# Performance work log

Hardware: AMD Instinct MI355X
Metric: run time of the kernel (lower is better)

Reference implementation:

```python
import jax, jax.numpy as jnp
import numpy as np

C = 256          # conv_channels
C1 = C // 2      # 128
C2 = C // 4      # 64
G = 1            # relation_glimpse


def setup_inputs() -> dict:
    key = jax.random.key(0)
    ks = jax.random.split(key, 20)
    bs, Nr, in_dim, q_dim = 4, 256, 2052, 1024
    d_in = in_dim + 4  # pos (first 4 coords) re-appended
    s = 0.02
    inp = {
        "Q": jax.random.normal(ks[0], (bs, q_dim), jnp.float32),
        "X": jax.random.normal(ks[1], (bs, Nr, in_dim), jnp.float32),
        "Wv": jax.random.normal(ks[2], (d_in, C), jnp.float32) * s,
        "bv": jnp.zeros((C,), jnp.float32),
        "Wq": jax.random.normal(ks[3], (q_dim, C), jnp.float32) * s,
        "bq": jnp.zeros((C,), jnp.float32),
        # branch 0 (r_conv01/02/03): 1x1 convs == per-position dense
        "W01": jax.random.normal(ks[4], (C, C1), jnp.float32) * s,
        "b01": jnp.zeros((C1,), jnp.float32),
        "W02": jax.random.normal(ks[5], (C1, C2), jnp.float32) * s,
        "b02": jnp.zeros((C2,), jnp.float32),
        "W03": jax.random.normal(ks[6], (C2, G), jnp.float32) * s,
        "b03": jnp.zeros((G,), jnp.float32),
        # branch 1 (r_conv1/2/3): dilation on 1x1 kernels is a no-op
        "W1": jax.random.normal(ks[7], (C, C1), jnp.float32) * s,
        "b1": jnp.zeros((C1,), jnp.float32),
        "W2": jax.random.normal(ks[8], (C1, C2), jnp.float32) * s,
        "b2": jnp.zeros((C2,), jnp.float32),
        "W3": jax.random.normal(ks[9], (C2, G), jnp.float32) * s,
        "b3": jnp.zeros((G,), jnp.float32),
    }
    return inp


def _mlp3(P, Wa, ba, Wb, bb, Wc, bc):
    # P: [bs, Nr, Nr, C]; three 1x1-conv layers, ReLU after each (incl. last).
    h = jax.nn.relu(jnp.einsum("bijc,ck->bijk", P, Wa) + ba)
    h = jax.nn.relu(jnp.einsum("bijc,ck->bijk", h, Wb) + bb)
    h = jax.nn.relu(jnp.einsum("bijc,ck->bijk", h, Wc) + bc)
    return h[..., 0]  # [bs, Nr, Nr] (relation_glimpse == 1)


def _attn_map(h):
    # symmetrize, then softmax over all Nr*Nr positions
    s = h + jnp.swapaxes(h, 1, 2)
    bs, Nr, _ = s.shape
    return jax.nn.softmax(s.reshape(bs, Nr * Nr), axis=-1).reshape(bs, Nr, Nr)


def reference(Q, X, Wv, bv, Wq, bq, W01, b01, W02, b02, W03, b03,
              W1, b1, W2, b2, W3, b3):
    X_ = X
    # append pos (first 4 coords) -> [bs, Nr, in_dim+4]
    Xcat = jnp.concatenate([X, X[:, :, :4]], axis=2)
    Xp = jnp.einsum("bnd,dc->bnc", Xcat, Wv) + bv
    Qp = Q @ Wq + bq
    Xp = Xp + Qp[:, None, :]                       # [bs, Nr, C]
    P = Xp[:, None, :, :] * Xp[:, :, None, :]      # [bs, Nr, Nr, C] pairwise product
    m0 = _attn_map(_mlp3(P, W01, b01, W02, b02, W03, b03))
    m1 = _attn_map(_mlp3(P, W1, b1, W2, b2, W3, b3))
    # weighted aggregation with original features; /(2*glimpse), then sum over Nr
    rel = jnp.einsum("bij,bjd->bid", m0 + m1, X_) / (2.0 * G)
    return rel.sum(axis=1)  # [bs, in_dim]
```

## Files before the change

kernel.cpp:

```cpp
#include <hip/hip_runtime.h>
#include <hip/hip_bf16.h>

typedef __attribute__((ext_vector_type(8)))  short short8;
typedef __attribute__((ext_vector_type(4)))  float f32x4;
typedef __attribute__((ext_vector_type(16))) float f32x16;

#define NR 256
#define CC 256

__device__ __forceinline__ unsigned short f2bf(float x) {
    union { float f; unsigned int u; } v; v.f = x;
    unsigned int r = v.u + 0x7FFFu + ((v.u >> 16) & 1u);
    return (unsigned short)(r >> 16);
}

__device__ __forceinline__ unsigned int pk2bf(float a, float b) {
    __hip_bfloat162 h = __float22bfloat162_rn(make_float2(a, b));
    union { __hip_bfloat162 h; unsigned int u; } cv; cv.h = h;
    return cv.u;
}

__global__ __launch_bounds__(256) void setup_kernel(
    const float* __restrict__ Q, const float* __restrict__ Wq, float* __restrict__ Qpp,
    const float* __restrict__ Wv, unsigned short* __restrict__ wvp,
    const float* __restrict__ W01, const float* __restrict__ W1,
    const float* __restrict__ W02, const float* __restrict__ W2,
    unsigned short* __restrict__ wpa, unsigned short* __restrict__ wpb)
{
    __shared__ float tile[32][260];
    __shared__ float qs[256];
    const int bx = blockIdx.x;
    const int tid = threadIdx.x;

    if (bx < 16) {
        int ksl = bx & 3, b = bx >> 2;
        qs[tid] = Q[b * 1024 + ksl * 256 + tid];
        __syncthreads();
        float acc = 0.f;
        #pragma unroll 4
        for (int d = 0; d < 256; ++d) acc += qs[d] * Wq[(size_t)(ksl * 256 + d) * 256 + tid];
        Qpp[(ksl * 4 + b) * 256 + tid] = acc;
    } else if (bx < 81) {
        int ks = bx - 16;
        for (int idx = tid; idx < 32 * 256; idx += 256) {
            int cr = idx >> 8, n = idx & 255;
            int c = ks * 32 + cr;
            tile[cr][n] = (c < 2056) ? Wv[(size_t)c * 256 + n] : 0.f;
        }
        __syncthreads();
        #pragma unroll
        for (int q = 0; q < 4; ++q) {
            int t2 = tid * 4 + q;
            int nt = t2 >> 6, l = t2 & 63;
            int gg = l >> 4, jj = l & 15;
            short8 s;
            #pragma unroll
            for (int e = 0; e < 8; ++e)
                s[e] = (short)f2bf(tile[gg * 8 + e][nt * 16 + jj]);
            *(short8*)&wvp[((size_t)(ks * 16 + nt) * 64 + l) * 8] = s;
        }
    } else {
        int t = (bx - 81) * 256 + tid;
        if (t < 65536) {
            int e = t & 7, l = (t >> 3) & 63, ks = (t >> 9) & 15, nt = (t >> 13) & 3, br = (t >> 15) & 1;
            int cc = ks * 16 + (l >> 5) * 8 + e;
            int n = nt * 32 + (l & 31);
            const float* W = br ? W1 : W01;
            wpa[t] = f2bf(W[cc * 128 + n]);
        } else {
            int t2 = t - 65536;
            int e = t2 & 7, l = (t2 >> 3) & 63, ks = (t2 >> 9) & 7, nt = (t2 >> 12) & 1, br = (t2 >> 13) & 1;
            int cc = ks * 16 + (l >> 5) * 8 + e;
            int n = nt * 32 + (l & 31);
            const float* W = br ? W2 : W02;
            wpb[t2] = f2bf(W[cc * 64 + n]);
        }
    }
}

__global__ __launch_bounds__(512) void xp_kernel(
    const float* __restrict__ X, const unsigned short* __restrict__ wvp,
    const float* __restrict__ bv, const float* __restrict__ bq,
    const float* __restrict__ Qpp, float* __restrict__ Xp)
{
    __shared__ f32x4 red[8][2][65];
    const int tid = threadIdx.x;
    const int w = tid >> 6;
    const int lane = tid & 63;
    const int g = lane >> 4, j16 = lane & 15;
    const int mt = blockIdx.x;
    const int bn = blockIdx.y;
    const int b  = blockIdx.z;

    const int i0 = mt * 16;
    const int n0 = bn * 32;
    const float* xrow = X + ((size_t)(b * NR) + (i0 + j16)) * 2052;

    f32x4 acc[2] = {};

    for (int ks = w; ks < 64; ks += 8) {
        const int c0 = ks * 32 + g * 8;
        float4 xa = *(const float4*)(xrow + c0);
        float4 xb = *(const float4*)(xrow + c0 + 4);
        union { short8 s; unsigned int u[4]; } af;
        af.u[0] = pk2bf(xa.x, xa.y);
        af.u[1] = pk2bf(xa.z, xa.w);
        af.u[2] = pk2bf(xb.x, xb.y);
        af.u[3] = pk2bf(xb.z, xb.w);
        #pragma unroll
        for (int nt = 0; nt < 2; ++nt) {
            short8 bf = ((const short8*)wvp)[(size_t)(ks * 16 + bn * 2 + nt) * 64 + lane];
            acc[nt] = __builtin_amdgcn_mfma_f32_16x16x32_bf16(af.s, bf, acc[nt], 0, 0, 0);
        }
    }
    if (w == 0) {
        float xv[8];
        #pragma unroll
        for (int e = 0; e < 8; ++e) {
            int q = g * 8 + e;
            int csrc = (q < 4) ? (2048 + q) : (q - 4);
            xv[e] = xrow[csrc];
        }
        union { short8 s; unsigned int u[4]; } af;
        af.u[0] = pk2bf(xv[0], xv[1]);
        af.u[1] = pk2bf(xv[2], xv[3]);
        af.u[2] = pk2bf(xv[4], xv[5]);
        af.u[3] = pk2bf(xv[6], xv[7]);
        #pragma unroll
        for (int nt = 0; nt < 2; ++nt) {
            short8 bf = ((const short8*)wvp)[(size_t)(64 * 16 + bn * 2 + nt) * 64 + lane];
            acc[nt] = __builtin_amdgcn_mfma_f32_16x16x32_bf16(af.s, bf, acc[nt], 0, 0, 0);
        }
    }
    #pragma unroll
    for (int nt = 0; nt < 2; ++nt) red[w][nt][lane] = acc[nt];
    __syncthreads();

    {
        int nt  = tid >> 8;
        int rem = tid & 255;
        int l   = rem & 63;
        int reg = (rem >> 6) & 3;
        float r = 0.f;
        #pragma unroll
        for (int ww = 0; ww < 8; ++ww) r += red[ww][nt][l][reg];
        int gg = l >> 4, jj = l & 15;
        int n = n0 + nt * 16 + jj;
        float base = bv[n] + bq[n] + Qpp[b * 256 + n] + Qpp[(4 + b) * 256 + n]
                   + Qpp[(8 + b) * 256 + n] + Qpp[(12 + b) * 256 + n];
        int row = i0 + gg * 4 + reg;
        Xp[((b * NR) + row) * CC + n] = r + base;
    }
}

__global__ __launch_bounds__(512, 2) void pairs_kernel(
    const float* __restrict__ Xp,
    const unsigned short* __restrict__ wpa,
    const unsigned short* __restrict__ wpb,
    const float* __restrict__ b01, const float* __restrict__ b02,
    const float* __restrict__ b03,
    const float* __restrict__ b1,  const float* __restrict__ b2,
    const float* __restrict__ b3,
    const float* __restrict__ W03, const float* __restrict__ W3,
    float* __restrict__ colpart, float* __restrict__ rowpart)
{
    __shared__ __align__(16) unsigned short lds_wa[32768];
    __shared__ __align__(16) float lds_si[2048];
    __shared__ __align__(16) float lds_bias1[128];
    __shared__ __align__(16) float lds_bias2[64];
    __shared__ __align__(16) float lds_w3[64];
    __shared__ float lds_c[8][33];

    const int tid = threadIdx.x;
    const int wave = tid >> 6;
    const int lane = tid & 63;
    const int hi = lane >> 5;
    const int j32 = lane & 31;

    int bx = blockIdx.x;
    int b = bx / 288;
    int r = bx - b * 288;
    int br = r / 144;
    int u = r - br * 144;
    int k = 0, off = 0;
    while (k < 7) {
        int cnt = 4 * (8 - k);
        if (u < off + cnt) break;
        off += cnt; ++k;
    }
    int rel = u - off;
    int it8 = 4 * k + rel / (8 - k);
    int jt  = k + rel % (8 - k);

    const int i = it8 * 8 + wave;
    const int blk = br * 4 + b;
    const int j0 = jt * 32;
    const int j = j0 + j32;

    *(float4*)&lds_si[wave * 256 + lane * 4] =
        *(const float4*)&Xp[((b * NR) + i) * CC + lane * 4];

    {
        const uint4* g1 = (const uint4*)(wpa + (size_t)br * 32768);
        uint4* s1 = (uint4*)lds_wa;
        #pragma unroll
        for (int kk = 0; kk < 8; ++kk) s1[kk * 512 + tid] = g1[kk * 512 + tid];
        if (tid < 128) lds_bias1[tid] = br ? b1[tid] : b01[tid];
        else if (tid < 192) lds_bias2[tid - 128] = br ? b2[tid - 128] : b02[tid - 128];
        else if (tid < 256) lds_w3[tid - 192] = br ? W3[tid - 192] : W03[tid - 192];
    }
    __syncthreads();
    const float b3v = br ? b3[0] : b03[0];
    const float* si = lds_si + wave * 256;

    const float* xr = Xp + ((size_t)(b * NR) + j) * CC;
    short8 bfr[16];
    #pragma unroll
    for (int ks = 0; ks < 16; ++ks) {
        const int c0 = ks * 16 + hi * 8;
        float4 xa = *(const float4*)(xr + c0);
        float4 xb = *(const float4*)(xr + c0 + 4);
        float4 sa = *(const float4*)(si + c0);
        float4 sb = *(const float4*)(si + c0 + 4);
        union { short8 s; unsigned int uu[4]; } f;
        f.uu[0] = pk2bf(xa.x * sa.x, xa.y * sa.y);
        f.uu[1] = pk2bf(xa.z * sa.z, xa.w * sa.w);
        f.uu[2] = pk2bf(xb.x * sb.x, xb.y * sb.y);
        f.uu[3] = pk2bf(xb.z * sb.z, xb.w * sb.w);
        bfr[ks] = f.s;
    }

    f32x16 acc1[4];
    #pragma unroll
    for (int t = 0; t < 4; ++t) {
        #pragma unroll
        for (int q = 0; q < 4; ++q) {
            const float* bb = &lds_bias1[t * 32 + q * 8 + hi * 4];
            acc1[t][q * 4 + 0] = bb[0];
            acc1[t][q * 4 + 1] = bb[1];
            acc1[t][q * 4 + 2] = bb[2];
            acc1[t][q * 4 + 3] = bb[3];
        }
    }
    #pragma unroll
    for (int ks = 0; ks < 16; ++ks) {
        const short8 bb = bfr[ks];
        #pragma unroll
        for (int t = 0; t < 4; ++t) {
            short8 wf = ((const short8*)lds_wa)[(t * 16 + ks) * 64 + lane];
            acc1[t] = __builtin_amdgcn_mfma_f32_32x32x16_bf16(wf, bb, acc1[t], 0, 0, 0);
        }
    }

    short8 w2r[16];
    {
        const short8* wb = (const short8*)wpb + (size_t)br * 1024;
        #pragma unroll
        for (int q = 0; q < 16; ++q) w2r[q] = wb[q * 64 + lane];
    }

    f32x16 acc2[2];
    #pragma unroll
    for (int nt = 0; nt < 2; ++nt) {
        #pragma unroll
        for (int q = 0; q < 4; ++q) {
            const float* bb = &lds_bias2[nt * 32 + q * 8 + hi * 4];
            acc2[nt][q * 4 + 0] = bb[0];
            acc2[nt][q * 4 + 1] = bb[1];
            acc2[nt][q * 4 + 2] = bb[2];
            acc2[nt][q * 4 + 3] = bb[3];
        }
    }
    #pragma unroll
    for (int t = 0; t < 4; ++t) {
        #pragma unroll
        for (int s = 0; s < 2; ++s) {
            const int bse = s * 8;
            float rA0 = fmaxf(acc1[t][bse + 0], 0.f), rA1 = fmaxf(acc1[t][bse + 1], 0.f);
            float rA2 = fmaxf(acc1[t][bse + 2], 0.f), rA3 = fmaxf(acc1[t][bse + 3], 0.f);
            float rB0 = fmaxf(acc1[t][bse + 4], 0.f), rB1 = fmaxf(acc1[t][bse + 5], 0.f);
            float rB2 = fmaxf(acc1[t][bse + 6], 0.f), rB3 = fmaxf(acc1[t][bse + 7], 0.f);
            unsigned int uA0 = pk2bf(rA0, rA1), uA1 = pk2bf(rA2, rA3);
            unsigned int uB0 = pk2bf(rB0, rB1), uB1 = pk2bf(rB2, rB3);
            unsigned int pA0 = __shfl_xor(uA0, 32, 64), pA1 = __shfl_xor(uA1, 32, 64);
            unsigned int pB0 = __shfl_xor(uB0, 32, 64), pB1 = __shfl_xor(uB1, 32, 64);
            union { short8 s8; unsigned int uu[4]; } B2;
            B2.uu[0] = hi ? pB0 : uA0;
            B2.uu[1] = hi ? pB1 : uA1;
            B2.uu[2] = hi ? uB0 : pA0;
            B2.uu[3] = hi ? uB1 : pA1;
            const int ks2 = 2 * t + s;
            acc2[0] = __builtin_amdgcn_mfma_f32_32x32x16_bf16(w2r[ks2], B2.s8, acc2[0], 0, 0, 0);
            acc2[1] = __builtin_amdgcn_mfma_f32_32x32x16_bf16(w2r[8 + ks2], B2.s8, acc2[1], 0, 0, 0);
        }
    }

    float part = 0.f;
    #pragma unroll
    for (int nt = 0; nt < 2; ++nt) {
        #pragma unroll
        for (int q = 0; q < 4; ++q) {
            const float* wv = &lds_w3[nt * 32 + q * 8 + hi * 4];
            part += fmaxf(acc2[nt][q * 4 + 0], 0.f) * wv[0];
            part += fmaxf(acc2[nt][q * 4 + 1], 0.f) * wv[1];
            part += fmaxf(acc2[nt][q * 4 + 2], 0.f) * wv[2];
            part += fmaxf(acc2[nt][q * 4 + 3], 0.f) * wv[3];
        }
    }
    part += __shfl_xor(part, 32, 64);
    const float h3 = fmaxf(part + b3v, 0.f);
    const float E = __expf(2.f * h3);
    const float Ec = (j >= i) ? E : 0.f;
    float Er = (j >  i) ? E : 0.f;

    Er += __shfl_xor(Er, 1, 64);
    Er += __shfl_xor(Er, 2, 64);
    Er += __shfl_xor(Er, 4, 64);
    Er += __shfl_xor(Er, 8, 64);
    Er += __shfl_xor(Er, 16, 64);
    Er += __shfl_xor(Er, 32, 64);
    if (lane == 0)
        rowpart[((size_t)blk * NR + i) * 8 + jt] = 0.5f * Er;

    if (!hi) lds_c[wave][j32] = Ec;
    __syncthreads();
    if (tid < 32) {
        float c = 0.f;
        #pragma unroll
        for (int w2 = 0; w2 < 8; ++w2) c += lds_c[w2][tid];
        colpart[(size_t)blk * 4608 + 64 * jt * (jt + 1) + tid * (4 * jt + 4) + it8] = c;
    }
}

__global__ __launch_bounds__(256) void colsoft_final_kernel(
    const float* __restrict__ colpart, const float* __restrict__ rowpart,
    float* __restrict__ wn)
{
    const int blk = blockIdx.x;
    const int j = threadIdx.x;
    const int jt = j >> 5, j32l = j & 31;
    const int cnt = 4 * jt + 4;
    float cs = 0.f;
    const float* cp = colpart + (size_t)blk * 4608 + 64 * jt * (jt + 1) + j32l * cnt;
    for (int it2 = 0; it2 < cnt; ++it2) cs += cp[it2];
    const float* rp = rowpart + ((size_t)blk * NR + j) * 8;
    for (int q = jt; q < 8; ++q) cs += rp[q];

    __shared__ float red[256];
    red[j] = cs; __syncthreads();
    for (int s = 128; s > 0; s >>= 1) {
        if (j < s) red[j] += red[j + s];
        __syncthreads();
    }
    wn[blk * 256 + j] = cs / red[0];
}

__global__ __launch_bounds__(256) void agg_part_kernel(
    const float* __restrict__ X, const float* __restrict__ wn,
    float* __restrict__ apart)
{
    const int dc = blockIdx.x, b = blockIdx.y, jc = blockIdx.z;
    const int d = dc * 256 + threadIdx.x;
    __shared__ float wc[32];
    if (threadIdx.x < 32) {
        int j = jc * 32 + threadIdx.x;
        wc[threadIdx.x] = 0.5f * (wn[b * 256 + j] + wn[(4 + b) * 256 + j]);
    }
    __syncthreads();
    if (d < 2052) {
        const float* xp = X + (size_t)b * NR * 2052 + (size_t)jc * 32 * 2052 + d;
        float a0 = 0.f, a1 = 0.f, a2 = 0.f, a3 = 0.f;
        for (int rr = 0; rr < 32; rr += 4) {
            a0 += wc[rr + 0] * xp[(size_t)(rr + 0) * 2052];
            a1 += wc[rr + 1] * xp[(size_t)(rr + 1) * 2052];
            a2 += wc[rr + 2] * xp[(size_t)(rr + 2) * 2052];
            a3 += wc[rr + 3] * xp[(size_t)(rr + 3) * 2052];
        }
        apart[(size_t)(jc * 4 + b) * 2304 + d] = (a0 + a1) + (a2 + a3);
    }
}

__global__ __launch_bounds__(256) void agg_final_kernel(
    const float* __restrict__ apart, float* __restrict__ out)
{
    const int dc = blockIdx.x, b = blockIdx.y;
    const int d = dc * 256 + threadIdx.x;
    if (d < 2052) {
        float s = 0.f;
        #pragma unroll
        for (int jc = 0; jc < 8; ++jc) s += apart[(size_t)(jc * 4 + b) * 2304 + d];
        out[b * 2052 + d] = s;
    }
}

extern "C" void kernel_launch(void* const* d_in, const int* in_sizes, int n_in,
                              void* d_out, int out_size, void* d_ws, size_t ws_size,
                              hipStream_t stream) {
    const float* Q   = (const float*)d_in[0];
    const float* X   = (const float*)d_in[1];
    const float* Wv  = (const float*)d_in[2];
    const float* bv  = (const float*)d_in[3];
    const float* Wq  = (const float*)d_in[4];
    const float* bq  = (const float*)d_in[5];
    const float* W01 = (const float*)d_in[6];
    const float* b01 = (const float*)d_in[7];
    const float* W02 = (const float*)d_in[8];
    const float* b02 = (const float*)d_in[9];
    const float* W03 = (const float*)d_in[10];
    const float* b03 = (const float*)d_in[11];
    const float* W1  = (const float*)d_in[12];
    const float* b1  = (const float*)d_in[13];
    const float* W2  = (const float*)d_in[14];
    const float* b2  = (const float*)d_in[15];
    const float* W3  = (const float*)d_in[16];
    const float* b3  = (const float*)d_in[17];

    char* ws = (char*)d_ws;
    float* Xp   = (float*)(ws + 0);
    float* Qpp  = (float*)(ws + 1048576);
    float* wn   = (float*)(ws + 1064960);
    unsigned short* wpa = (unsigned short*)(ws + 1073152);
    unsigned short* wpb = (unsigned short*)(ws + 1204224);
    float* colpart = (float*)(ws + 1236992);
    float* rowpart = (float*)(ws + 1384448);
    unsigned short* wvp = (unsigned short*)(ws + 1236992);
    float* apart = (float*)(ws + 0);
    float* out = (float*)d_out;

    setup_kernel<<<401, 256, 0, stream>>>(Q, Wq, Qpp, Wv, wvp,
                                          W01, W1, W02, W2, wpa, wpb);
    xp_kernel<<<dim3(16, 8, 4), 512, 0, stream>>>(X, wvp, bv, bq, Qpp, Xp);
    pairs_kernel<<<1152, 512, 0, stream>>>(Xp, wpa, wpb, b01, b02, b03,
                                           b1, b2, b3, W03, W3, colpart, rowpart);
    colsoft_final_kernel<<<8, 256, 0, stream>>>(colpart, rowpart, wn);
    agg_part_kernel<<<dim3(9, 4, 8), 256, 0, stream>>>(X, wn, apart);
    agg_final_kernel<<<dim3(9, 4), 256, 0, stream>>>(apart, out);
}
```

Measured before the change: 91.93 us.

## Switch pairs MLP to 16x16 MFMA tiles, merge softmax normalization into aggregation

The pairs kernel now uses 16x16x32 MFMA with 16-column j tiles instead of 32x32x16. It streams the first-layer weights into LDS in two halves and keeps the second-layer weights in LDS rather than registers, which shrinks LDS and register footprint and doubles the block count. The xp kernel computes 128 output columns per block (fewer blocks, more reuse of X loads). The separate column-softmax kernel is removed and its normalization is recomputed redundantly inside each aggregation block, saving one launch at the cost of duplicated reductions.

```diff
diff --git a/kernel.cpp b/kernel.cpp
--- a/kernel.cpp
+++ b/kernel.cpp
@@ -3,7 +3,6 @@
 
 typedef __attribute__((ext_vector_type(8)))  short short8;
 typedef __attribute__((ext_vector_type(4)))  float f32x4;
-typedef __attribute__((ext_vector_type(16))) float f32x16;
 
 #define NR 256
 #define CC 256
@@ -62,16 +61,16 @@
     } else {
         int t = (bx - 81) * 256 + tid;
         if (t < 65536) {
-            int e = t & 7, l = (t >> 3) & 63, ks = (t >> 9) & 15, nt = (t >> 13) & 3, br = (t >> 15) & 1;
-            int cc = ks * 16 + (l >> 5) * 8 + e;
-            int n = nt * 32 + (l & 31);
+            int e = t & 7, l = (t >> 3) & 63, ks = (t >> 9) & 7, nt = (t >> 12) & 7, br = (t >> 15) & 1;
+            int cc = ks * 32 + (l >> 4) * 8 + e;
+            int n = nt * 16 + (l & 15);
             const float* W = br ? W1 : W01;
             wpa[t] = f2bf(W[cc * 128 + n]);
         } else {
             int t2 = t - 65536;
-            int e = t2 & 7, l = (t2 >> 3) & 63, ks = (t2 >> 9) & 7, nt = (t2 >> 12) & 1, br = (t2 >> 13) & 1;
-            int cc = ks * 16 + (l >> 5) * 8 + e;
-            int n = nt * 32 + (l & 31);
+            int e = t2 & 7, l = (t2 >> 3) & 63, ks = (t2 >> 9) & 3, nt = (t2 >> 11) & 3, br = (t2 >> 13) & 1;
+            int cc = ks * 32 + (l >> 4) * 8 + e;
+            int n = nt * 16 + (l & 15);
             const float* W = br ? W2 : W02;
             wpb[t2] = f2bf(W[cc * 64 + n]);
         }
@@ -83,20 +82,19 @@
     const float* __restrict__ bv, const float* __restrict__ bq,
     const float* __restrict__ Qpp, float* __restrict__ Xp)
 {
-    __shared__ f32x4 red[8][2][65];
+    __shared__ f32x4 red[8][8][65];
     const int tid = threadIdx.x;
     const int w = tid >> 6;
     const int lane = tid & 63;
-    const int g = lane >> 4, j16 = lane & 15;
+    const int g = lane >> 4, j16v = lane & 15;
     const int mt = blockIdx.x;
-    const int bn = blockIdx.y;
+    const int bn2 = blockIdx.y;
     const int b  = blockIdx.z;
 
     const int i0 = mt * 16;
-    const int n0 = bn * 32;
-    const float* xrow = X + ((size_t)(b * NR) + (i0 + j16)) * 2052;
-
-    f32x4 acc[2] = {};
+    const float* xrow = X + ((size_t)(b * NR) + (i0 + j16v)) * 2052;
+
+    f32x4 acc[8] = {};
 
     for (int ks = w; ks < 64; ks += 8) {
         const int c0 = ks * 32 + g * 8;
@@ -108,8 +106,8 @@
         af.u[2] = pk2bf(xb.x, xb.y);
         af.u[3] = pk2bf(xb.z, xb.w);
         #pragma unroll
-        for (int nt = 0; nt < 2; ++nt) {
-            short8 bf = ((const short8*)wvp)[(size_t)(ks * 16 + bn * 2 + nt) * 64 + lane];
+        for (int nt = 0; nt < 8; ++nt) {
+            short8 bf = ((const short8*)wvp)[(size_t)(ks * 16 + bn2 * 8 + nt) * 64 + lane];
             acc[nt] = __builtin_amdgcn_mfma_f32_16x16x32_bf16(af.s, bf, acc[nt], 0, 0, 0);
         }
     }
@@ -127,29 +125,27 @@
         af.u[2] = pk2bf(xv[4], xv[5]);
         af.u[3] = pk2bf(xv[6], xv[7]);
         #pragma unroll
-        for (int nt = 0; nt < 2; ++nt) {
-            short8 bf = ((const short8*)wvp)[(size_t)(64 * 16 + bn * 2 + nt) * 64 + lane];
+        for (int nt = 0; nt < 8; ++nt) {
+            short8 bf = ((const short8*)wvp)[(size_t)(64 * 16 + bn2 * 8 + nt) * 64 + lane];
             acc[nt] = __builtin_amdgcn_mfma_f32_16x16x32_bf16(af.s, bf, acc[nt], 0, 0, 0);
         }
     }
     #pragma unroll
-    for (int nt = 0; nt < 2; ++nt) red[w][nt][lane] = acc[nt];
-    __syncthreads();
-
-    {
-        int nt  = tid >> 8;
-        int rem = tid & 255;
-        int l   = rem & 63;
-        int reg = (rem >> 6) & 3;
-        float r = 0.f;
-        #pragma unroll
-        for (int ww = 0; ww < 8; ++ww) r += red[ww][nt][l][reg];
+    for (int nt = 0; nt < 8; ++nt) red[w][nt][lane] = acc[nt];
+    __syncthreads();
+
+    for (int idx = tid; idx < 2048; idx += 512) {
+        int nt = idx >> 8, rem = idx & 255;
+        int l = rem & 63, reg = rem >> 6;
+        float rsum = 0.f;
+        #pragma unroll
+        for (int ww = 0; ww < 8; ++ww) rsum += red[ww][nt][l][reg];
         int gg = l >> 4, jj = l & 15;
-        int n = n0 + nt * 16 + jj;
+        int n = bn2 * 128 + nt * 16 + jj;
         float base = bv[n] + bq[n] + Qpp[b * 256 + n] + Qpp[(4 + b) * 256 + n]
                    + Qpp[(8 + b) * 256 + n] + Qpp[(12 + b) * 256 + n];
         int row = i0 + gg * 4 + reg;
-        Xp[((b * NR) + row) * CC + n] = r + base;
+        Xp[((b * NR) + row) * CC + n] = rsum + base;
     }
 }
 
@@ -164,60 +160,68 @@
     const float* __restrict__ W03, const float* __restrict__ W3,
     float* __restrict__ colpart, float* __restrict__ rowpart)
 {
-    __shared__ __align__(16) unsigned short lds_wa[32768];
+    __shared__ __align__(16) unsigned short lds_wa[16384];
+    __shared__ __align__(16) unsigned short lds_wb[8192];
     __shared__ __align__(16) float lds_si[2048];
     __shared__ __align__(16) float lds_bias1[128];
     __shared__ __align__(16) float lds_bias2[64];
     __shared__ __align__(16) float lds_w3[64];
-    __shared__ float lds_c[8][33];
+    __shared__ float lds_c[8][17];
 
     const int tid = threadIdx.x;
     const int wave = tid >> 6;
     const int lane = tid & 63;
-    const int hi = lane >> 5;
-    const int j32 = lane & 31;
+    const int g = lane >> 4;
+    const int j16 = lane & 15;
 
     int bx = blockIdx.x;
-    int b = bx / 288;
-    int r = bx - b * 288;
-    int br = r / 144;
-    int u = r - br * 144;
+    int b = bx / 544;
+    int r = bx - b * 544;
+    int br = r / 272;
+    int u = r - br * 272;
     int k = 0, off = 0;
-    while (k < 7) {
-        int cnt = 4 * (8 - k);
+    while (k < 15) {
+        int cnt = 2 * (16 - k);
         if (u < off + cnt) break;
         off += cnt; ++k;
     }
-    int rel = u - off;
-    int it8 = 4 * k + rel / (8 - k);
-    int jt  = k + rel % (8 - k);
+    int rel = u - off, wdt = 16 - k;
+    int it8 = 2 * k + rel / wdt;
+    int jt16 = k + rel % wdt;
 
     const int i = it8 * 8 + wave;
     const int blk = br * 4 + b;
-    const int j0 = jt * 32;
-    const int j = j0 + j32;
+    const int j = jt16 * 16 + j16;
 
     *(float4*)&lds_si[wave * 256 + lane * 4] =
         *(const float4*)&Xp[((b * NR) + i) * CC + lane * 4];
 
+    const uint4* gwa = (const uint4*)wpa + (size_t)br * 4096;
+
     {
-        const uint4* g1 = (const uint4*)(wpa + (size_t)br * 32768);
         uint4* s1 = (uint4*)lds_wa;
         #pragma unroll
-        for (int kk = 0; kk < 8; ++kk) s1[kk * 512 + tid] = g1[kk * 512 + tid];
+        for (int it = 0; it < 4; ++it) {
+            int q = it * 512 + tid;
+            int nt = q >> 8, ksl = (q >> 6) & 3, le = q & 63;
+            s1[q] = gwa[(nt * 8 + ksl) * 64 + le];
+        }
+        const uint4* g2 = (const uint4*)wpb + (size_t)br * 1024;
+        uint4* s2 = (uint4*)lds_wb;
+        s2[tid] = g2[tid];
+        s2[512 + tid] = g2[512 + tid];
         if (tid < 128) lds_bias1[tid] = br ? b1[tid] : b01[tid];
         else if (tid < 192) lds_bias2[tid - 128] = br ? b2[tid - 128] : b02[tid - 128];
         else if (tid < 256) lds_w3[tid - 192] = br ? W3[tid - 192] : W03[tid - 192];
     }
-    __syncthreads();
     const float b3v = br ? b3[0] : b03[0];
     const float* si = lds_si + wave * 256;
-
     const float* xr = Xp + ((size_t)(b * NR) + j) * CC;
-    short8 bfr[16];
-    #pragma unroll
-    for (int ks = 0; ks < 16; ++ks) {
-        const int c0 = ks * 16 + hi * 8;
+
+    short8 bfr[4];
+    #pragma unroll
+    for (int ksl = 0; ksl < 4; ++ksl) {
+        const int c0 = ksl * 32 + g * 8;
         float4 xa = *(const float4*)(xr + c0);
         float4 xb = *(const float4*)(xr + c0 + 4);
         float4 sa = *(const float4*)(si + c0);
@@ -227,87 +231,106 @@
         f.uu[1] = pk2bf(xa.z * sa.z, xa.w * sa.w);
         f.uu[2] = pk2bf(xb.x * sb.x, xb.y * sb.y);
         f.uu[3] = pk2bf(xb.z * sb.z, xb.w * sb.w);
-        bfr[ks] = f.s;
-    }
-
-    f32x16 acc1[4];
+        bfr[ksl] = f.s;
+    }
+    __syncthreads();
+
+    f32x4 acc1[8];
+    #pragma unroll
+    for (int nt = 0; nt < 8; ++nt)
+        acc1[nt] = *(const f32x4*)&lds_bias1[nt * 16 + g * 4];
+
+    #pragma unroll
+    for (int ksl = 0; ksl < 4; ++ksl) {
+        const short8 bb = bfr[ksl];
+        #pragma unroll
+        for (int nt = 0; nt < 8; ++nt) {
+            short8 wf = ((const short8*)lds_wa)[(nt * 4 + ksl) * 64 + lane];
+            acc1[nt] = __builtin_amdgcn_mfma_f32_16x16x32_bf16(wf, bb, acc1[nt], 0, 0, 0);
+        }
+    }
+    __syncthreads();
+
+    {
+        uint4* s1 = (uint4*)lds_wa;
+        #pragma unroll
+        for (int it = 0; it < 4; ++it) {
+            int q = it * 512 + tid;
+            int nt = q >> 8, ksl = (q >> 6) & 3, le = q & 63;
+            s1[q] = gwa[(nt * 8 + 4 + ksl) * 64 + le];
+        }
+    }
+    #pragma unroll
+    for (int ksl = 0; ksl < 4; ++ksl) {
+        const int c0 = 128 + ksl * 32 + g * 8;
+        float4 xa = *(const float4*)(xr + c0);
+        float4 xb = *(const float4*)(xr + c0 + 4);
+        float4 sa = *(const float4*)(si + c0);
+        float4 sb = *(const float4*)(si + c0 + 4);
+        union { short8 s; unsigned int uu[4]; } f;
+        f.uu[0] = pk2bf(xa.x * sa.x, xa.y * sa.y);
+        f.uu[1] = pk2bf(xa.z * sa.z, xa.w * sa.w);
+        f.uu[2] = pk2bf(xb.x * sb.x, xb.y * sb.y);
+        f.uu[3] = pk2bf(xb.z * sb.z, xb.w * sb.w);
+        bfr[ksl] = f.s;
+    }
+    __syncthreads();
+
+    #pragma unroll
+    for (int ksl = 0; ksl < 4; ++ksl) {
+        const short8 bb = bfr[ksl];
+        #pragma unroll
+        for (int nt = 0; nt < 8; ++nt) {
+            short8 wf = ((const short8*)lds_wa)[(nt * 4 + ksl) * 64 + lane];
+            acc1[nt] = __builtin_amdgcn_mfma_f32_16x16x32_bf16(wf, bb, acc1[nt], 0, 0, 0);
+        }
+    }
+
+    f32x4 acc2[4];
+    #pragma unroll
+    for (int nt2 = 0; nt2 < 4; ++nt2)
+        acc2[nt2] = *(const f32x4*)&lds_bias2[nt2 * 16 + g * 4];
+
+    const int sl0 = ((lane & 16) ? 32 : 0) + j16;
+    const int sl1 = sl0 + 16;
+    const bool hiL = (g >> 1);
+
     #pragma unroll
     for (int t = 0; t < 4; ++t) {
-        #pragma unroll
-        for (int q = 0; q < 4; ++q) {
-            const float* bb = &lds_bias1[t * 32 + q * 8 + hi * 4];
-            acc1[t][q * 4 + 0] = bb[0];
-            acc1[t][q * 4 + 1] = bb[1];
-            acc1[t][q * 4 + 2] = bb[2];
-            acc1[t][q * 4 + 3] = bb[3];
-        }
-    }
-    #pragma unroll
-    for (int ks = 0; ks < 16; ++ks) {
-        const short8 bb = bfr[ks];
-        #pragma unroll
-        for (int t = 0; t < 4; ++t) {
-            short8 wf = ((const short8*)lds_wa)[(t * 16 + ks) * 64 + lane];
-            acc1[t] = __builtin_amdgcn_mfma_f32_32x32x16_bf16(wf, bb, acc1[t], 0, 0, 0);
-        }
-    }
-
-    short8 w2r[16];
-    {
-        const short8* wb = (const short8*)wpb + (size_t)br * 1024;
-        #pragma unroll
-        for (int q = 0; q < 16; ++q) w2r[q] = wb[q * 64 + lane];
-    }
-
-    f32x16 acc2[2];
-    #pragma unroll
-    for (int nt = 0; nt < 2; ++nt) {
-        #pragma unroll
-        for (int q = 0; q < 4; ++q) {
-            const float* bb = &lds_bias2[nt * 32 + q * 8 + hi * 4];
-            acc2[nt][q * 4 + 0] = bb[0];
-            acc2[nt][q * 4 + 1] = bb[1];
-            acc2[nt][q * 4 + 2] = bb[2];
-            acc2[nt][q * 4 + 3] = bb[3];
-        }
-    }
-    #pragma unroll
-    for (int t = 0; t < 4; ++t) {
-        #pragma unroll
-        for (int s = 0; s < 2; ++s) {
-            const int bse = s * 8;
-            float rA0 = fmaxf(acc1[t][bse + 0], 0.f), rA1 = fmaxf(acc1[t][bse + 1], 0.f);
-            float rA2 = fmaxf(acc1[t][bse + 2], 0.f), rA3 = fmaxf(acc1[t][bse + 3], 0.f);
-            float rB0 = fmaxf(acc1[t][bse + 4], 0.f), rB1 = fmaxf(acc1[t][bse + 5], 0.f);
-            float rB2 = fmaxf(acc1[t][bse + 6], 0.f), rB3 = fmaxf(acc1[t][bse + 7], 0.f);
-            unsigned int uA0 = pk2bf(rA0, rA1), uA1 = pk2bf(rA2, rA3);
-            unsigned int uB0 = pk2bf(rB0, rB1), uB1 = pk2bf(rB2, rB3);
-            unsigned int pA0 = __shfl_xor(uA0, 32, 64), pA1 = __shfl_xor(uA1, 32, 64);
-            unsigned int pB0 = __shfl_xor(uB0, 32, 64), pB1 = __shfl_xor(uB1, 32, 64);
-            union { short8 s8; unsigned int uu[4]; } B2;
-            B2.uu[0] = hi ? pB0 : uA0;
-            B2.uu[1] = hi ? pB1 : uA1;
-            B2.uu[2] = hi ? uB0 : pA0;
-            B2.uu[3] = hi ? uB1 : pA1;
-            const int ks2 = 2 * t + s;
-            acc2[0] = __builtin_amdgcn_mfma_f32_32x32x16_bf16(w2r[ks2], B2.s8, acc2[0], 0, 0, 0);
-            acc2[1] = __builtin_amdgcn_mfma_f32_32x32x16_bf16(w2r[8 + ks2], B2.s8, acc2[1], 0, 0, 0);
+        float e0 = fmaxf(acc1[2*t][0], 0.f),   e1 = fmaxf(acc1[2*t][1], 0.f);
+        float e2 = fmaxf(acc1[2*t][2], 0.f),   e3 = fmaxf(acc1[2*t][3], 0.f);
+        float o0 = fmaxf(acc1[2*t+1][0], 0.f), o1 = fmaxf(acc1[2*t+1][1], 0.f);
+        float o2 = fmaxf(acc1[2*t+1][2], 0.f), o3 = fmaxf(acc1[2*t+1][3], 0.f);
+        unsigned int uE0 = pk2bf(e0, e1), uE1 = pk2bf(e2, e3);
+        unsigned int uO0 = pk2bf(o0, o1), uO1 = pk2bf(o2, o3);
+        unsigned int aE0 = __shfl(uE0, sl0, 64), aO0 = __shfl(uO0, sl0, 64);
+        unsigned int aE1 = __shfl(uE1, sl0, 64), aO1 = __shfl(uO1, sl0, 64);
+        unsigned int bE0 = __shfl(uE0, sl1, 64), bO0 = __shfl(uO0, sl1, 64);
+        unsigned int bE1 = __shfl(uE1, sl1, 64), bO1 = __shfl(uO1, sl1, 64);
+        union { short8 s8; unsigned int uu[4]; } B2;
+        B2.uu[0] = hiL ? aO0 : aE0;
+        B2.uu[1] = hiL ? aO1 : aE1;
+        B2.uu[2] = hiL ? bO0 : bE0;
+        B2.uu[3] = hiL ? bO1 : bE1;
+        #pragma unroll
+        for (int nt2 = 0; nt2 < 4; ++nt2) {
+            short8 wf2 = ((const short8*)lds_wb)[(nt2 * 4 + t) * 64 + lane];
+            acc2[nt2] = __builtin_amdgcn_mfma_f32_16x16x32_bf16(wf2, B2.s8, acc2[nt2], 0, 0, 0);
         }
     }
 
     float part = 0.f;
     #pragma unroll
-    for (int nt = 0; nt < 2; ++nt) {
-        #pragma unroll
-        for (int q = 0; q < 4; ++q) {
-            const float* wv = &lds_w3[nt * 32 + q * 8 + hi * 4];
-            part += fmaxf(acc2[nt][q * 4 + 0], 0.f) * wv[0];
-            part += fmaxf(acc2[nt][q * 4 + 1], 0.f) * wv[1];
-            part += fmaxf(acc2[nt][q * 4 + 2], 0.f) * wv[2];
-            part += fmaxf(acc2[nt][q * 4 + 3], 0.f) * wv[3];
-        }
-    }
+    for (int nt2 = 0; nt2 < 4; ++nt2) {
+        f32x4 wv = *(const f32x4*)&lds_w3[nt2 * 16 + g * 4];
+        part += fmaxf(acc2[nt2][0], 0.f) * wv[0];
+        part += fmaxf(acc2[nt2][1], 0.f) * wv[1];
+        part += fmaxf(acc2[nt2][2], 0.f) * wv[2];
+        part += fmaxf(acc2[nt2][3], 0.f) * wv[3];
+    }
+    part += __shfl_xor(part, 16, 64);
     part += __shfl_xor(part, 32, 64);
+
     const float h3 = fmaxf(part + b3v, 0.f);
     const float E = __expf(2.f * h3);
     const float Ec = (j >= i) ? E : 0.f;
@@ -320,53 +343,55 @@
     Er += __shfl_xor(Er, 16, 64);
     Er += __shfl_xor(Er, 32, 64);
     if (lane == 0)
-        rowpart[((size_t)blk * NR + i) * 8 + jt] = 0.5f * Er;
-
-    if (!hi) lds_c[wave][j32] = Ec;
-    __syncthreads();
-    if (tid < 32) {
+        rowpart[((size_t)blk * NR + i) * 16 + jt16] = 0.25f * Er;
+
+    if (lane < 16) lds_c[wave][lane] = Ec;
+    __syncthreads();
+    if (tid < 16) {
         float c = 0.f;
         #pragma unroll
         for (int w2 = 0; w2 < 8; ++w2) c += lds_c[w2][tid];
-        colpart[(size_t)blk * 4608 + 64 * jt * (jt + 1) + tid * (4 * jt + 4) + it8] = c;
-    }
-}
-
-__global__ __launch_bounds__(256) void colsoft_final_kernel(
-    const float* __restrict__ colpart, const float* __restrict__ rowpart,
-    float* __restrict__ wn)
-{
-    const int blk = blockIdx.x;
-    const int j = threadIdx.x;
-    const int jt = j >> 5, j32l = j & 31;
-    const int cnt = 4 * jt + 4;
-    float cs = 0.f;
-    const float* cp = colpart + (size_t)blk * 4608 + 64 * jt * (jt + 1) + j32l * cnt;
-    for (int it2 = 0; it2 < cnt; ++it2) cs += cp[it2];
-    const float* rp = rowpart + ((size_t)blk * NR + j) * 8;
-    for (int q = jt; q < 8; ++q) cs += rp[q];
-
-    __shared__ float red[256];
-    red[j] = cs; __syncthreads();
-    for (int s = 128; s > 0; s >>= 1) {
-        if (j < s) red[j] += red[j + s];
-        __syncthreads();
-    }
-    wn[blk * 256 + j] = cs / red[0];
+        colpart[(size_t)blk * 4352 + 16 * jt16 * (jt16 + 1) + tid * (2 * jt16 + 2) + it8] = c;
+    }
 }
 
 __global__ __launch_bounds__(256) void agg_part_kernel(
-    const float* __restrict__ X, const float* __restrict__ wn,
-    float* __restrict__ apart)
+    const float* __restrict__ X, const float* __restrict__ colpart,
+    const float* __restrict__ rowpart, float* __restrict__ apart)
 {
     const int dc = blockIdx.x, b = blockIdx.y, jc = blockIdx.z;
-    const int d = dc * 256 + threadIdx.x;
+    const int tid = threadIdx.x;
+    __shared__ float csh[2][256];
+    __shared__ float red2[2][256];
     __shared__ float wc[32];
-    if (threadIdx.x < 32) {
-        int j = jc * 32 + threadIdx.x;
-        wc[threadIdx.x] = 0.5f * (wn[b * 256 + j] + wn[(4 + b) * 256 + j]);
-    }
-    __syncthreads();
+
+    {
+        const int jt16 = tid >> 4, j16l = tid & 15;
+        const int cnt = 2 * jt16 + 2;
+        #pragma unroll
+        for (int brx = 0; brx < 2; ++brx) {
+            const int blk = brx * 4 + b;
+            float cs = 0.f;
+            const float* cp = colpart + (size_t)blk * 4352 + 16 * jt16 * (jt16 + 1) + j16l * cnt;
+            for (int it2 = 0; it2 < cnt; ++it2) cs += cp[it2];
+            const float* rp = rowpart + ((size_t)blk * NR + tid) * 16;
+            for (int q = jt16; q < 16; ++q) cs += rp[q];
+            csh[brx][tid] = cs;
+            red2[brx][tid] = cs;
+        }
+    }
+    __syncthreads();
+    for (int s = 128; s > 0; s >>= 1) {
+        if (tid < s) { red2[0][tid] += red2[0][tid + s]; red2[1][tid] += red2[1][tid + s]; }
+        __syncthreads();
+    }
+    if (tid < 32) {
+        int jx = jc * 32 + tid;
+        wc[tid] = 0.5f * (csh[0][jx] / red2[0][0] + csh[1][jx] / red2[1][0]);
+    }
+    __syncthreads();
+
+    const int d = dc * 256 + tid;
     if (d < 2052) {
         const float* xp = X + (size_t)b * NR * 2052 + (size_t)jc * 32 * 2052 + d;
         float a0 = 0.f, a1 = 0.f, a2 = 0.f, a3 = 0.f;
@@ -418,21 +443,19 @@
     char* ws = (char*)d_ws;
     float* Xp   = (float*)(ws + 0);
     float* Qpp  = (float*)(ws + 1048576);
-    float* wn   = (float*)(ws + 1064960);
     unsigned short* wpa = (unsigned short*)(ws + 1073152);
     unsigned short* wpb = (unsigned short*)(ws + 1204224);
     float* colpart = (float*)(ws + 1236992);
-    float* rowpart = (float*)(ws + 1384448);
+    float* rowpart = (float*)(ws + 1376256);
     unsigned short* wvp = (unsigned short*)(ws + 1236992);
     float* apart = (float*)(ws + 0);
     float* out = (float*)d_out;
 
     setup_kernel<<<401, 256, 0, stream>>>(Q, Wq, Qpp, Wv, wvp,
                                           W01, W1, W02, W2, wpa, wpb);
-    xp_kernel<<<dim3(16, 8, 4), 512, 0, stream>>>(X, wvp, bv, bq, Qpp, Xp);
-    pairs_kernel<<<1152, 512, 0, stream>>>(Xp, wpa, wpb, b01, b02, b03,
+    xp_kernel<<<dim3(16, 2, 4), 512, 0, stream>>>(X, wvp, bv, bq, Qpp, Xp);
+    pairs_kernel<<<2176, 512, 0, stream>>>(Xp, wpa, wpb, b01, b02, b03,
                                            b1, b2, b3, W03, W3, colpart, rowpart);
-    colsoft_final_kernel<<<8, 256, 0, stream>>>(colpart, rowpart, wn);
-    agg_part_kernel<<<dim3(9, 4, 8), 256, 0, stream>>>(X, wn, apart);
+    agg_part_kernel<<<dim3(9, 4, 8), 256, 0, stream>>>(X, colpart, rowpart, apart);
     agg_final_kernel<<<dim3(9, 4), 256, 0, stream>>>(apart, out);
 }
```

Result: slower. 106.1 us (+15.5%).
